# Kernel optimization log

Measured on AMD Instinct MI355X. Metric: run time of the kernel, lower is better.

## Reference

```python
import jax, jax.numpy as jnp
from jax import lax
import numpy as np

B, T, D, H = 512, 512, 128, 64


def setup_inputs() -> dict:
    key = jax.random.key(0)
    k_x, k_wi, k_wh, k_bi, k_bh = jax.random.split(key, 5)
    s = 1.0 / np.sqrt(H)  # torch LSTM init scale
    return {
        "x": jax.random.normal(k_x, (B, T, D), dtype=jnp.float32),
        "W_ih": jax.random.uniform(k_wi, (4 * H, D), minval=-s, maxval=s, dtype=jnp.float32),
        "W_hh": jax.random.uniform(k_wh, (4 * H, H), minval=-s, maxval=s, dtype=jnp.float32),
        "b_ih": jax.random.uniform(k_bi, (4 * H,), minval=-s, maxval=s, dtype=jnp.float32),
        "b_hh": jax.random.uniform(k_bh, (4 * H,), minval=-s, maxval=s, dtype=jnp.float32),
    }


def reference(x, W_ih, W_hh, b_ih, b_hh):
    # x: [B, T, D]; torch LSTM gate order: i, f, g, o
    Bv, Tv, _ = x.shape
    Hv = W_hh.shape[1]
    # Precompute all input-to-gate projections in one big GEMM: [B, T, 4H]
    xg = jnp.einsum("btd,gd->btg", x, W_ih) + b_ih + b_hh
    xg_t = jnp.swapaxes(xg, 0, 1)  # [T, B, 4H] for scan over time

    def step(carry, xt):
        h, c = carry
        gates = xt + h @ W_hh.T  # [B, 4H]
        i, f, g, o = jnp.split(gates, 4, axis=-1)
        i = jax.nn.sigmoid(i)
        f = jax.nn.sigmoid(f)
        g = jnp.tanh(g)
        o = jax.nn.sigmoid(o)
        c = f * c + i * g
        h = o * jnp.tanh(c)
        return (h, c), None

    h0 = jnp.zeros((Bv, Hv), dtype=x.dtype)
    (h_last, _), _ = lax.scan(step, (h0, h0), xg_t)
    return h_last  # out[:, -1, :] == final hidden state of a single-layer LSTM
```

## Files before the change

### kernel.cpp

```cpp
#include <hip/hip_runtime.h>
#include <hip/hip_fp16.h>
#include <math.h>


#define Bsz   512
#define Tlen  512
#define Din   128
#define Hdim  64
#define NGATE 256

typedef __attribute__((ext_vector_type(8))) short short8v;
typedef __attribute__((ext_vector_type(4))) float f32x4;
typedef __attribute__((ext_vector_type(2))) _Float16 h2v;
typedef unsigned short ushort_t;
typedef unsigned int uint_t;
typedef __attribute__((ext_vector_type(4))) uint_t uint4v;

__device__ __forceinline__ unsigned short f2bf_bits(float f) {
    union { float f; unsigned u; } v; v.f = f;
    unsigned r = v.u + 0x7fff + ((v.u >> 16) & 1);
    return (unsigned short)(r >> 16);
}
__device__ __forceinline__ float bf2f(unsigned short b) {
    union { unsigned u; float f; } v; v.u = ((unsigned)b) << 16;
    return v.f;
}
__device__ __forceinline__ uint_t pkh(float a, float b) {
    return (uint_t)__half_as_ushort(__float2half(a)) |
           ((uint_t)__half_as_ushort(__float2half(b)) << 16);
}
__device__ __forceinline__ h2v as_h2(uint_t u) {
    union { uint_t u; h2v h; } v; v.u = u; return v.h;
}
__device__ __forceinline__ float f16lo(uint_t u) {
    return __half2float(__ushort_as_half((ushort_t)(u & 0xffff)));
}
__device__ __forceinline__ float f16hi(uint_t u) {
    return __half2float(__ushort_as_half((ushort_t)(u >> 16)));
}
__device__ __forceinline__ float sigmoid_f(float v) {
    return 1.0f / (1.0f + __expf(-v));
}
__device__ __forceinline__ float tanh_f(float v) {
    float a = fabsf(v);
    float e = __expf(2.0f * a);
    float r = 1.0f - 2.0f / (e + 1.0f);
    return copysignf(r, v);
}

#if defined(__has_builtin)
#if __has_builtin(__builtin_amdgcn_fdot2)
#define FDOT2(a, b, c) __builtin_amdgcn_fdot2((a), (b), (c), false)
#endif
#endif
#ifndef FDOT2
#define FDOT2(a, b, c) fmaf((float)(a)[1], (float)(b)[1], fmaf((float)(a)[0], (float)(b)[0], (c)))
#endif

#define MF(acc, a, b) acc = __builtin_amdgcn_mfma_f32_16x16x32_bf16(a, b, acc, 0, 0, 0)

__global__ __launch_bounds__(256, 1)
void xg_gemm2(const float* __restrict__ x, const float* __restrict__ W_ih,
              const float* __restrict__ b_ih, const float* __restrict__ b_hh,
              uint_t* __restrict__ xg)
{
    __shared__ __align__(16) ushort_t sxh[2][16][136];
    __shared__ __align__(16) ushort_t sxl[2][16][136];

    const int tid = threadIdx.x;
    const int l = tid & 63, q = tid >> 6;
    const int jl = l & 15, s4 = l >> 4;
    const int rb = blockIdx.x & 31, tc = blockIdx.x >> 5;
    const int t0 = tc * 32;

    short8v wb[4][4];
    #pragma unroll
    for (int tt = 0; tt < 4; ++tt) {
        #pragma unroll
        for (int kt = 0; kt < 4; ++kt) {
            const float* wp = W_ih + (size_t)(tt * 64 + q * 16 + jl) * Din + kt * 32 + s4 * 8;
            f32x4 v0 = *(const f32x4*)wp;
            f32x4 v1 = *(const f32x4*)(wp + 4);
            #pragma unroll
            for (int j = 0; j < 8; ++j)
                wb[tt][kt][j] = (short)f2bf_bits((j < 4) ? v0[j] : v1[j - 4]);
        }
    }
    float bias[4];
    #pragma unroll
    for (int tt = 0; tt < 4; ++tt) {
        int g = tt * 64 + q * 16 + jl;
        bias[tt] = b_ih[g] + b_hh[g];
    }

    const int srow = tid >> 4, spart = tid & 15;
    const float* xrow = x + (size_t)(rb * 16 + srow) * Tlen * Din + spart * 8;
    f32x4 xr0 = *(const f32x4*)(xrow + (size_t)t0 * Din);
    f32x4 xr1 = *(const f32x4*)(xrow + (size_t)t0 * Din + 4);

    for (int ti = 0; ti < 32; ++ti) {
        const int t = t0 + ti, buf = ti & 1;

        short8v vh, vl;
        #pragma unroll
        for (int j = 0; j < 8; ++j) {
            float f = (j < 4) ? xr0[j] : xr1[j - 4];
            unsigned short hb = f2bf_bits(f);
            vh[j] = (short)hb;
            vl[j] = (short)f2bf_bits(f - bf2f(hb));
        }
        *(short8v*)&sxh[buf][srow][spart * 8] = vh;
        *(short8v*)&sxl[buf][srow][spart * 8] = vl;
        __syncthreads();

        if (ti + 1 < 32) {
            xr0 = *(const f32x4*)(xrow + (size_t)(t + 1) * Din);
            xr1 = *(const f32x4*)(xrow + (size_t)(t + 1) * Din + 4);
        }

        f32x4 acc0 = {0.f, 0.f, 0.f, 0.f}, acc1 = acc0, acc2 = acc0, acc3 = acc0;
        #pragma unroll
        for (int kt = 0; kt < 4; ++kt) {
            short8v ah = *(const short8v*)&sxh[buf][jl][kt * 32 + s4 * 8];
            short8v al = *(const short8v*)&sxl[buf][jl][kt * 32 + s4 * 8];
            MF(acc0, ah, wb[0][kt]); MF(acc1, ah, wb[1][kt]);
            MF(acc2, ah, wb[2][kt]); MF(acc3, ah, wb[3][kt]);
            MF(acc0, al, wb[0][kt]); MF(acc1, al, wb[1][kt]);
            MF(acc2, al, wb[2][kt]); MF(acc3, al, wb[3][kt]);
        }

        #pragma unroll
        for (int r = 0; r < 4; ++r) {
            const int brow = rb * 16 + s4 * 4 + r;
            uint2 st;
            st.x = pkh(acc0[r] + bias[0], acc1[r] + bias[1]);
            st.y = pkh(acc2[r] + bias[2], acc3[r] + bias[3]);
            *(uint2*)(xg + ((size_t)brow * Tlen + t) * 128 + (q * 16 + jl) * 2) = st;
        }
    }
}

__global__ __launch_bounds__(64) __attribute__((amdgpu_waves_per_eu(1, 1)))
void lstm_rec5(const uint_t* __restrict__ xg, const float* __restrict__ W_hh,
               float* __restrict__ out)
{
    __shared__ __align__(16) ushort_t hsh[Hdim];
    const int j = threadIdx.x;
    const int b = blockIdx.x;

    uint4v Wq[32];
    #pragma unroll
    for (int tt = 0; tt < 4; ++tt) {
        const float* wr = W_hh + (size_t)(tt * Hdim + j) * Hdim;
        #pragma unroll
        for (int qq = 0; qq < 8; ++qq) {
            #pragma unroll
            for (int c = 0; c < 4; ++c) {
                float2 w = *(const float2*)(wr + 8 * qq + 2 * c);
                Wq[tt * 8 + qq][c] = pkh(w.x, w.y);
            }
        }
    }

    hsh[j] = 0;
    asm volatile("" ::: "memory");
    float c = 0.0f, h = 0.0f;

    const uint_t* xp = xg + (size_t)b * (Tlen * 128) + j * 2;
    uint2 xcur = *(const uint2*)xp;
    uint2 xnxt = *(const uint2*)(xp + 128);

    for (int t = 0; t < Tlen; ++t) {
        uint4v hq[8];
        {
            const uint4v* hp = (const uint4v*)hsh;
            #pragma unroll
            for (int i = 0; i < 8; ++i) hq[i] = hp[i];
        }

        const int tn = (t + 2 < Tlen) ? t + 2 : Tlen - 1;
        uint2 xpf = *(const uint2*)(xp + (size_t)tn * 128);

        float gi0 = f16lo(xcur.x), gf0 = f16hi(xcur.x);
        float gg0 = f16lo(xcur.y), go0 = f16hi(xcur.y);
        float gi1 = 0.f, gf1 = 0.f, gg1 = 0.f, go1 = 0.f;
        #pragma unroll
        for (int qq = 0; qq < 8; ++qq) {
            h2v hx = as_h2(hq[qq][0]), hy = as_h2(hq[qq][1]);
            h2v hz = as_h2(hq[qq][2]), hw = as_h2(hq[qq][3]);
            gi0 = FDOT2(hx, as_h2(Wq[     qq][0]), gi0);
            gi1 = FDOT2(hy, as_h2(Wq[     qq][1]), gi1);
            gi0 = FDOT2(hz, as_h2(Wq[     qq][2]), gi0);
            gi1 = FDOT2(hw, as_h2(Wq[     qq][3]), gi1);
            gf0 = FDOT2(hx, as_h2(Wq[ 8 + qq][0]), gf0);
            gf1 = FDOT2(hy, as_h2(Wq[ 8 + qq][1]), gf1);
            gf0 = FDOT2(hz, as_h2(Wq[ 8 + qq][2]), gf0);
            gf1 = FDOT2(hw, as_h2(Wq[ 8 + qq][3]), gf1);
            gg0 = FDOT2(hx, as_h2(Wq[16 + qq][0]), gg0);
            gg1 = FDOT2(hy, as_h2(Wq[16 + qq][1]), gg1);
            gg0 = FDOT2(hz, as_h2(Wq[16 + qq][2]), gg0);
            gg1 = FDOT2(hw, as_h2(Wq[16 + qq][3]), gg1);
            go0 = FDOT2(hx, as_h2(Wq[24 + qq][0]), go0);
            go1 = FDOT2(hy, as_h2(Wq[24 + qq][1]), go1);
            go0 = FDOT2(hz, as_h2(Wq[24 + qq][2]), go0);
            go1 = FDOT2(hw, as_h2(Wq[24 + qq][3]), go1);
        }

        float iv = sigmoid_f(gi0 + gi1);
        float fv = sigmoid_f(gf0 + gf1);
        float gv = tanh_f(gg0 + gg1);
        float ov = sigmoid_f(go0 + go1);
        c = fv * c + iv * gv;
        h = ov * tanh_f(c);

        hsh[j] = __half_as_ushort(__float2half(h));
        asm volatile("" ::: "memory");

        xcur = xnxt;
        xnxt = xpf;
    }

    out[(size_t)b * Hdim + j] = h;
}

#define LDS_DWORDS 33920
__global__ void __launch_bounds__(256, 1)
lstm_fused(const float* __restrict__ x, const float* __restrict__ W_ih,
           const float* __restrict__ W_hh, const float* __restrict__ b_ih,
           const float* __restrict__ b_hh, float* __restrict__ out)
{
    extern __shared__ float lds[];
    float* wih   = lds;
    float* xbuf  = lds + 32768;
    float* gates = lds + 33280;
    float* hbuf  = lds + 33792;

    const int tid = threadIdx.x;
    const int g   = tid;
    const int row_base = blockIdx.x * 2;

    {
        const float4* src = reinterpret_cast<const float4*>(W_ih);
        float4* dst = reinterpret_cast<float4*>(wih);
        #pragma unroll
        for (int i = 0; i < 32; ++i) {
            int qq = i * 256 + tid;
            int rg = qq >> 5;
            int cc = qq & 31;
            dst[rg * 32 + (cc ^ (rg & 7))] = src[qq];
        }
    }
    float4 whh[16];
    {
        const float4* src = reinterpret_cast<const float4*>(W_hh) + g * 16;
        #pragma unroll
        for (int cc = 0; cc < 16; ++cc) whh[cc] = src[cc];
    }
    const float bias = b_ih[g] + b_hh[g];
    if (tid < 128) hbuf[tid] = 0.0f;
    {
        int r = tid >> 7, k = tid & 127;
        xbuf[tid] = x[((size_t)(row_base + r) * Tlen + 0) * Din + k];
    }
    float cstate = 0.0f, hval = 0.0f;
    __syncthreads();

    int cur = 0;
    const int sw = g & 7;
    const float4* w4 = reinterpret_cast<const float4*>(wih) + g * 32;

    for (int t = 0; t < Tlen; ++t) {
        float xnext = 0.0f;
        if (t + 1 < Tlen) {
            int r = tid >> 7, k = tid & 127;
            xnext = x[((size_t)(row_base + r) * Tlen + (t + 1)) * Din + k];
        }
        float acc0 = bias, acc1 = bias;
        {
            const float4* xr0 = reinterpret_cast<const float4*>(xbuf + cur * 256);
            const float4* xr1 = reinterpret_cast<const float4*>(xbuf + cur * 256 + 128);
            #pragma unroll 8
            for (int cc = 0; cc < 32; ++cc) {
                float4 w = w4[cc ^ sw];
                float4 a = xr0[cc];
                float4 bb = xr1[cc];
                acc0 += w.x * a.x + w.y * a.y + w.z * a.z + w.w * a.w;
                acc1 += w.x * bb.x + w.y * bb.y + w.z * bb.z + w.w * bb.w;
            }
        }
        {
            const float4* h0 = reinterpret_cast<const float4*>(hbuf);
            const float4* h1 = reinterpret_cast<const float4*>(hbuf + 64);
            #pragma unroll
            for (int cc = 0; cc < 16; ++cc) {
                float4 w = whh[cc];
                float4 a = h0[cc];
                float4 bb = h1[cc];
                acc0 += w.x * a.x + w.y * a.y + w.z * a.z + w.w * a.w;
                acc1 += w.x * bb.x + w.y * bb.y + w.z * bb.z + w.w * bb.w;
            }
        }
        gates[g]       = acc0;
        gates[256 + g] = acc1;
        __syncthreads();

        if (tid < 128) {
            int r = tid >> 6, jj = tid & 63;
            const float* gr = gates + r * 256;
            float ig = sigmoid_f(gr[jj]);
            float fg = sigmoid_f(gr[64 + jj]);
            float gg = tanh_f(gr[128 + jj]);
            float og = sigmoid_f(gr[192 + jj]);
            cstate = fg * cstate + ig * gg;
            hval   = og * tanh_f(cstate);
            hbuf[r * 64 + jj] = hval;
        }
        if (t + 1 < Tlen) xbuf[(cur ^ 1) * 256 + tid] = xnext;
        __syncthreads();
        cur ^= 1;
    }
    if (tid < 128) {
        int r = tid >> 6, jj = tid & 63;
        out[(size_t)(row_base + r) * Hdim + jj] = hval;
    }
}

extern "C" void kernel_launch(void* const* d_in, const int* in_sizes, int n_in,
                              void* d_out, int out_size, void* d_ws, size_t ws_size,
                              hipStream_t stream) {
    const float* x    = (const float*)d_in[0];
    const float* W_ih = (const float*)d_in[1];
    const float* W_hh = (const float*)d_in[2];
    const float* b_ih = (const float*)d_in[3];
    const float* b_hh = (const float*)d_in[4];
    float* out = (float*)d_out;

    const size_t need = (size_t)Bsz * Tlen * NGATE * 2;
    if (ws_size >= need) {
        uint_t* xgws = (uint_t*)d_ws;
        xg_gemm2<<<512, 256, 0, stream>>>(x, W_ih, b_ih, b_hh, xgws);
        lstm_rec5<<<Bsz, 64, 0, stream>>>(xgws, W_hh, out);
    } else {
        const size_t lds_bytes = (size_t)LDS_DWORDS * 4;
        hipFuncSetAttribute(reinterpret_cast<const void*>(lstm_fused),
                            hipFuncAttributeMaxDynamicSharedMemorySize, (int)lds_bytes);
        lstm_fused<<<Bsz / 2, 256, lds_bytes, stream>>>(x, W_ih, W_hh, b_ih, b_hh, out);
    }
}
```

Baseline: 320.4 us.

## Split LSTM recurrence gates across four waves with LDS gate exchange

The recurrent kernel now launches 256 threads per batch row instead of 64, with one wave per gate (i, f, g, o). Each wave holds only its gate's W_hh slice in registers and computes one dot product per hidden unit per step. The activated gates are exchanged through a double-buffered shared array behind one barrier per timestep. Every wave then recomputes c and h redundantly into its own h copy, so no second barrier is needed. This shortens the serial per-step work and register footprint, at the cost of a block-wide barrier and LDS traffic on every step.

```diff
diff --git a/kernel.cpp b/kernel.cpp
--- a/kernel.cpp
+++ b/kernel.cpp
@@ -140,87 +140,84 @@
     }
 }
 
-__global__ __launch_bounds__(64) __attribute__((amdgpu_waves_per_eu(1, 1)))
-void lstm_rec5(const uint_t* __restrict__ xg, const float* __restrict__ W_hh,
+__global__ __launch_bounds__(256, 1)
+void lstm_rec6(const uint_t* __restrict__ xg, const float* __restrict__ W_hh,
                float* __restrict__ out)
 {
-    __shared__ __align__(16) ushort_t hsh[Hdim];
-    const int j = threadIdx.x;
-    const int b = blockIdx.x;
-
-    uint4v Wq[32];
-    #pragma unroll
-    for (int tt = 0; tt < 4; ++tt) {
-        const float* wr = W_hh + (size_t)(tt * Hdim + j) * Hdim;
+    __shared__ float    gsh[2][4][Hdim];
+    __shared__ __align__(16) ushort_t hsh[4][Hdim];
+
+    const int tid = threadIdx.x;
+    const int j  = tid & 63;
+    const int tt = tid >> 6;
+
+    uint4v Wq[8];
+    {
+        const float2* wr = (const float2*)(W_hh + (size_t)(tt * Hdim + j) * Hdim);
         #pragma unroll
         for (int qq = 0; qq < 8; ++qq) {
             #pragma unroll
-            for (int c = 0; c < 4; ++c) {
-                float2 w = *(const float2*)(wr + 8 * qq + 2 * c);
-                Wq[tt * 8 + qq][c] = pkh(w.x, w.y);
+            for (int cc = 0; cc < 4; ++cc) {
+                float2 w = wr[qq * 4 + cc];
+                Wq[qq][cc] = pkh(w.x, w.y);
             }
         }
     }
 
-    hsh[j] = 0;
+    hsh[tt][j] = 0;
     asm volatile("" ::: "memory");
     float c = 0.0f, h = 0.0f;
 
-    const uint_t* xp = xg + (size_t)b * (Tlen * 128) + j * 2;
-    uint2 xcur = *(const uint2*)xp;
-    uint2 xnxt = *(const uint2*)(xp + 128);
+    const int b = blockIdx.x;
+    const uint_t* xp = xg + (size_t)b * (Tlen * 128) + j * 2 + (tt >> 1);
+    uint_t xcur = xp[0];
+    uint_t xnxt = xp[128];
+
+    const uint4v* hp = (const uint4v*)&hsh[tt][0];
 
     for (int t = 0; t < Tlen; ++t) {
+        const int buf = t & 1;
+
         uint4v hq[8];
-        {
-            const uint4v* hp = (const uint4v*)hsh;
-            #pragma unroll
-            for (int i = 0; i < 8; ++i) hq[i] = hp[i];
-        }
+        #pragma unroll
+        for (int i = 0; i < 8; ++i) hq[i] = hp[i];
 
         const int tn = (t + 2 < Tlen) ? t + 2 : Tlen - 1;
-        uint2 xpf = *(const uint2*)(xp + (size_t)tn * 128);
-
-        float gi0 = f16lo(xcur.x), gf0 = f16hi(xcur.x);
-        float gg0 = f16lo(xcur.y), go0 = f16hi(xcur.y);
-        float gi1 = 0.f, gf1 = 0.f, gg1 = 0.f, go1 = 0.f;
+        uint_t xpf = xp[(size_t)tn * 128];
+
+        float a0 = (tt & 1) ? f16hi(xcur) : f16lo(xcur);
+        float a1 = 0.f, a2 = 0.f, a3 = 0.f;
         #pragma unroll
         for (int qq = 0; qq < 8; ++qq) {
-            h2v hx = as_h2(hq[qq][0]), hy = as_h2(hq[qq][1]);
-            h2v hz = as_h2(hq[qq][2]), hw = as_h2(hq[qq][3]);
-            gi0 = FDOT2(hx, as_h2(Wq[     qq][0]), gi0);
-            gi1 = FDOT2(hy, as_h2(Wq[     qq][1]), gi1);
-            gi0 = FDOT2(hz, as_h2(Wq[     qq][2]), gi0);
-            gi1 = FDOT2(hw, as_h2(Wq[     qq][3]), gi1);
-            gf0 = FDOT2(hx, as_h2(Wq[ 8 + qq][0]), gf0);
-            gf1 = FDOT2(hy, as_h2(Wq[ 8 + qq][1]), gf1);
-            gf0 = FDOT2(hz, as_h2(Wq[ 8 + qq][2]), gf0);
-            gf1 = FDOT2(hw, as_h2(Wq[ 8 + qq][3]), gf1);
-            gg0 = FDOT2(hx, as_h2(Wq[16 + qq][0]), gg0);
-            gg1 = FDOT2(hy, as_h2(Wq[16 + qq][1]), gg1);
-            gg0 = FDOT2(hz, as_h2(Wq[16 + qq][2]), gg0);
-            gg1 = FDOT2(hw, as_h2(Wq[16 + qq][3]), gg1);
-            go0 = FDOT2(hx, as_h2(Wq[24 + qq][0]), go0);
-            go1 = FDOT2(hy, as_h2(Wq[24 + qq][1]), go1);
-            go0 = FDOT2(hz, as_h2(Wq[24 + qq][2]), go0);
-            go1 = FDOT2(hw, as_h2(Wq[24 + qq][3]), go1);
-        }
-
-        float iv = sigmoid_f(gi0 + gi1);
-        float fv = sigmoid_f(gf0 + gf1);
-        float gv = tanh_f(gg0 + gg1);
-        float ov = sigmoid_f(go0 + go1);
+            a0 = FDOT2(as_h2(hq[qq][0]), as_h2(Wq[qq][0]), a0);
+            a1 = FDOT2(as_h2(hq[qq][1]), as_h2(Wq[qq][1]), a1);
+            a2 = FDOT2(as_h2(hq[qq][2]), as_h2(Wq[qq][2]), a2);
+            a3 = FDOT2(as_h2(hq[qq][3]), as_h2(Wq[qq][3]), a3);
+        }
+        float pre = (a0 + a1) + (a2 + a3);
+
+        float act;
+        if (tt == 2) act = tanh_f(pre);
+        else         act = sigmoid_f(pre);
+
+        gsh[buf][tt][j] = act;
+        __syncthreads();
+
+        float iv = gsh[buf][0][j];
+        float fv = gsh[buf][1][j];
+        float gv = gsh[buf][2][j];
+        float ov = gsh[buf][3][j];
         c = fv * c + iv * gv;
         h = ov * tanh_f(c);
 
-        hsh[j] = __half_as_ushort(__float2half(h));
+        hsh[tt][j] = __half_as_ushort(__float2half(h));
         asm volatile("" ::: "memory");
 
         xcur = xnxt;
         xnxt = xpf;
     }
 
-    out[(size_t)b * Hdim + j] = h;
+    if (tt == 0) out[(size_t)b * Hdim + j] = h;
 }
 
 #define LDS_DWORDS 33920
@@ -339,7 +336,7 @@
     if (ws_size >= need) {
         uint_t* xgws = (uint_t*)d_ws;
         xg_gemm2<<<512, 256, 0, stream>>>(x, W_ih, b_ih, b_hh, xgws);
-        lstm_rec5<<<Bsz, 64, 0, stream>>>(xgws, W_hh, out);
+        lstm_rec6<<<Bsz, 256, 0, stream>>>(xgws, W_hh, out);
     } else {
         const size_t lds_bytes = (size_t)LDS_DWORDS * 4;
         hipFuncSetAttribute(reinterpret_cast<const void*>(lstm_fused),
```

New measurement: 308.3 us. 1.04x faster.
